# Kernel tuning notes

Hardware: AMD Instinct MI355X
Metric: run time of the kernel (lower is better)

The kernel has to match this reference:

```python
import jax, jax.numpy as jnp
import numpy as np

N_HEAD = 8
N_FEAT = 512
EPS = 1e-6


def _forward(query, Wq, bq, Wk, bk, Wv, bv, Wo, bo):
    # query: (bsz, tgt_len, E). key = value = query (self-attention).
    bsz, tgt_len, E = query.shape
    head_dim = E // N_HEAD
    n = bsz * N_HEAD

    # Faithful to torch: .view((L, N, E)) is a RESHAPE, not a transpose.
    x = query.reshape(tgt_len, bsz, E)

    q = x @ Wq.T + bq
    k = x @ Wk.T + bk
    v = x @ Wv.T + bv

    # relu activation on q, k (act_fun='relu')
    q = jax.nn.relu(q).reshape(tgt_len, n, head_dim).swapaxes(0, 1)  # (n, L, d)
    k = jax.nn.relu(k).reshape(tgt_len, n, head_dim).swapaxes(0, 1)  # (n, L, d)
    v = v.reshape(tgt_len, n, head_dim).swapaxes(0, 1)               # (n, L, d)

    # cos reweighting: weight_index = pi/2 * arange(1, m+1) / m
    m = tgt_len
    idx = (np.pi / 2) * jnp.arange(1, m + 1, dtype=query.dtype) / m  # (L,)
    idx = idx[None, :, None]                                         # (1, L, 1)
    q_ = jnp.concatenate([q * jnp.sin(idx), q * jnp.cos(idx)], axis=-1)  # (n, L, 2d)
    k_ = jnp.concatenate([k * jnp.sin(idx), k * jnp.cos(idx)], axis=-1)  # (n, L, 2d)

    # causal linear attention via cumsum recurrence
    kv = jnp.einsum('nld,nlm->nldm', k_, v)          # (n, L, 2d, d)
    kv_cum = jnp.cumsum(kv, axis=1)                  # (n, L, 2d, d)
    qkv = jnp.einsum('nld,nldm->nlm', q_, kv_cum)    # (n, L, d)
    k_cum = jnp.cumsum(k_, axis=1)                   # (n, L, 2d)
    denom = jnp.clip(jnp.einsum('nld,nld->nl', q_, k_cum), EPS, None)
    attn = qkv / denom[..., None]                    # (n, L, d)

    attn = attn.swapaxes(0, 1).reshape(tgt_len, bsz, E)
    out = attn @ Wo.T + bo
    # Faithful to torch: final .view back to (bsz, tgt_len, E) is a reshape.
    return out.reshape(bsz, tgt_len, N_FEAT)


def setup_inputs() -> dict:
    key = jax.random.key(0)
    ks = jax.random.split(key, 9)
    bsz, L, E = 2, 1024, N_FEAT
    scale = 0.02
    return {
        'query': jax.random.normal(ks[0], (bsz, L, E), dtype=jnp.float32),
        'Wq': jax.random.normal(ks[1], (E, E), dtype=jnp.float32) * scale,
        'bq': jnp.zeros((E,), dtype=jnp.float32),
        'Wk': jax.random.normal(ks[2], (E, E), dtype=jnp.float32) * scale,
        'bk': jnp.zeros((E,), dtype=jnp.float32),
        'Wv': jax.random.normal(ks[3], (E, E), dtype=jnp.float32) * scale,
        'bv': jnp.zeros((E,), dtype=jnp.float32),
        'Wo': jax.random.normal(ks[4], (E, E), dtype=jnp.float32) * scale,
        'bo': jnp.zeros((E,), dtype=jnp.float32),
    }


def reference(query, Wq, bq, Wk, bk, Wv, bv, Wo, bo):
    return _forward(query, Wq, bq, Wk, bk, Wv, bv, Wo, bo)
```

## Files before the change

### kernel.cpp

```cpp
#include <hip/hip_runtime.h>
#include <math.h>

#define LSEQ 1024
#define EDIM 512
#define HD 64
#define CCH 32
#define NCH 32
#define DFEAT 128

typedef unsigned short u16;
typedef short bf16x8 __attribute__((ext_vector_type(8)));
typedef float f32x4 __attribute__((ext_vector_type(4)));

__device__ __forceinline__ u16 f2bf(float f) {
    unsigned u = __float_as_uint(f);
    unsigned r = (u + 0x7fffu + ((u >> 16) & 1u)) >> 16;
    return (u16)r;
}
__device__ __forceinline__ float bf2f(u16 x) {
    return __uint_as_float((unsigned)x << 16);
}
__device__ __forceinline__ void async16(void* lds, const void* g) {
    __builtin_amdgcn_global_load_lds(
        (const __attribute__((address_space(1))) unsigned int*)g,
        (__attribute__((address_space(3))) unsigned int*)lds, 16, 0, 0);
}

__global__ __launch_bounds__(256) void cast_kernel(
    const float* __restrict__ X,  const float* __restrict__ Wq,
    const float* __restrict__ Wk, const float* __restrict__ Wv,
    const float* __restrict__ Wo, u16* __restrict__ Xb, u16* __restrict__ Wb)
{
    int i = blockIdx.x * 256 + threadIdx.x;
    const float* src; u16* dst; int off;
    if (i < 262144)      { src = X;  dst = Xb;          off = i; }
    else if (i < 327680) { src = Wq; dst = Wb;          off = i - 262144; }
    else if (i < 393216) { src = Wk; dst = Wb + 262144; off = i - 327680; }
    else if (i < 458752) { src = Wv; dst = Wb + 524288; off = i - 393216; }
    else                 { src = Wo; dst = Wb + 786432; off = i - 458752; }
    float4 v = *(const float4*)&src[(size_t)off * 4];
    ushort4 o; o.x = f2bf(v.x); o.y = f2bf(v.y); o.z = f2bf(v.z); o.w = f2bf(v.w);
    *(ushort4*)&dst[(size_t)off * 4] = o;
}

__global__ __launch_bounds__(256) void qkv_mfma_kernel(
    const u16* __restrict__ Xb, const u16* __restrict__ Wb,
    const float* __restrict__ bq, const float* __restrict__ bk, const float* __restrict__ bv,
    u16* __restrict__ qf, u16* __restrict__ kf, u16* __restrict__ vf)
{
    const int z = blockIdx.z;
    const u16* __restrict__ W = Wb + (size_t)z * 262144;
    const float* __restrict__ bias = (z == 0) ? bq : (z == 1) ? bk : bv;
    const int r0 = blockIdx.x * 128;
    const int j0 = blockIdx.y * 128;
    __shared__ u16 As[128 * 32];
    __shared__ u16 Bs[128 * 32];
    const int t = threadIdx.x;
    const int wave = t >> 6, lane = t & 63;
    const int wm = (wave & 1) * 64, wn = (wave >> 1) * 64;
    const int cl = lane & 15, rg4 = lane >> 4;
    f32x4 acc[4][4];
    #pragma unroll
    for (int fi = 0; fi < 4; ++fi)
        #pragma unroll
        for (int fj = 0; fj < 4; ++fj) acc[fi][fj] = (f32x4){0.f, 0.f, 0.f, 0.f};

    for (int kb = 0; kb < 512; kb += 32) {
        #pragma unroll
        for (int i = 0; i < 2; ++i) {
            int chunk = i * 256 + t;
            int row = chunk >> 2, kg = chunk & 3;
            async16(&As[(size_t)(i * 256 + wave * 64) * 8], Xb + (size_t)(r0 + row) * 512 + kb + kg * 8);
            async16(&Bs[(size_t)(i * 256 + wave * 64) * 8], W  + (size_t)(j0 + row) * 512 + kb + kg * 8);
        }
        __syncthreads();
        bf16x8 af[4], bg[4];
        #pragma unroll
        for (int f = 0; f < 4; ++f) {
            af[f] = *(const bf16x8*)&As[(wm + f * 16 + cl) * 32 + rg4 * 8];
            bg[f] = *(const bf16x8*)&Bs[(wn + f * 16 + cl) * 32 + rg4 * 8];
        }
        #pragma unroll
        for (int fi = 0; fi < 4; ++fi)
            #pragma unroll
            for (int fj = 0; fj < 4; ++fj)
                acc[fi][fj] = __builtin_amdgcn_mfma_f32_16x16x32_bf16(af[fi], bg[fj], acc[fi][fj], 0, 0, 0);
        __syncthreads();
    }

    float biasv[4];
    #pragma unroll
    for (int fj = 0; fj < 4; ++fj) biasv[fj] = bias[j0 + wn + fj * 16 + cl];
    #pragma unroll
    for (int fi = 0; fi < 4; ++fi) {
        #pragma unroll
        for (int rr = 0; rr < 4; ++rr) {
            const int row_g = r0 + wm + fi * 16 + rg4 * 4 + rr;
            const int l = row_g >> 1, bb = row_g & 1;
            if (z < 2) {
                float ang = 1.5707963267948966f * (float)(l + 1) * (1.0f / 1024.0f);
                float sv, cv;
                sincosf(ang, &sv, &cv);
                u16* __restrict__ dst = (z == 0) ? qf : kf;
                #pragma unroll
                for (int fj = 0; fj < 4; ++fj) {
                    const int jg = j0 + wn + fj * 16 + cl;
                    float y = fmaxf(acc[fi][fj][rr] + biasv[fj], 0.f);
                    const int h = jg >> 6, d = jg & 63;
                    size_t base = (size_t)((bb * 8 + h) * LSEQ + l) * DFEAT;
                    dst[base + d]      = f2bf(y * sv);
                    dst[base + d + 64] = f2bf(y * cv);
                }
            } else {
                #pragma unroll
                for (int fj = 0; fj < 4; ++fj) {
                    const int jg = j0 + wn + fj * 16 + cl;
                    float y = acc[fi][fj][rr] + biasv[fj];
                    const int h = jg >> 6, d = jg & 63;
                    vf[(size_t)((bb * 8 + h) * LSEQ + l) * HD + d] = f2bf(y);
                }
            }
        }
    }
}

__global__ __launch_bounds__(256) void chunk_sum_kernel(
    const u16* __restrict__ kf, const u16* __restrict__ vf,
    float* __restrict__ KVc, float* __restrict__ K1c)
{
    const int n = blockIdx.x >> 5;
    const int c = blockIdx.x & 31;
    __shared__ u16 Ks[32 * 128];
    __shared__ u16 VT[64 * 32];
    const int t = threadIdx.x;
    const int wave = t >> 6, lane = t & 63;
    const int cl = lane & 15, rg4 = lane >> 4;
    const u16* kbase = kf + (size_t)(n * LSEQ + c * CCH) * DFEAT;
    const u16* vbase = vf + (size_t)(n * LSEQ + c * CCH) * HD;
    #pragma unroll
    for (int i = 0; i < 2; ++i)
        async16(&Ks[(size_t)(i * 256 + wave * 64) * 8], kbase + (size_t)(i * 256 + t) * 8);
    {
        u16 tmp[8];
        #pragma unroll
        for (int j = 0; j < 8; ++j) tmp[j] = vbase[(wave * 8 + j) * HD + lane];
        *(bf16x8*)&VT[lane * 32 + wave * 8] = *(bf16x8*)tmp;
    }
    __syncthreads();

    bf16x8 af = *(const bf16x8*)&VT[(wave * 16 + cl) * 32 + rg4 * 8];
    f32x4 acc[8];
    #pragma unroll
    for (int ni = 0; ni < 8; ++ni) {
        u16 bt[8];
        #pragma unroll
        for (int j = 0; j < 8; ++j)
            bt[j] = Ks[(rg4 * 8 + j) * 128 + ni * 16 + cl];
        acc[ni] = __builtin_amdgcn_mfma_f32_16x16x32_bf16(af, *(bf16x8*)bt,
                                                          (f32x4){0.f,0.f,0.f,0.f}, 0, 0, 0);
    }
    float* out = KVc + (size_t)(n * NCH + c) * (HD * DFEAT);
    #pragma unroll
    for (int ni = 0; ni < 8; ++ni)
        #pragma unroll
        for (int r = 0; r < 4; ++r) {
            int m = wave * 16 + rg4 * 4 + r;
            out[(size_t)m * 128 + ni * 16 + cl] = acc[ni][r];
        }
    if (t < 128) {
        float s = 0.f;
        #pragma unroll
        for (int l = 0; l < 32; ++l) s += bf2f(Ks[l * 128 + t]);
        K1c[(size_t)(n * NCH + c) * DFEAT + t] = s;
    }
}

__global__ __launch_bounds__(256) void prefix_kernel(
    const float* __restrict__ KVc, const float* __restrict__ K1c,
    u16* __restrict__ Spt, float* __restrict__ K1p)
{
    const int bx = blockIdx.x, t = threadIdx.x;
    if (bx < 512) {
        const int n = bx >> 5;
        const int e = (bx & 31) * 256 + t;
        const float* src = KVc + (size_t)n * NCH * 8192 + e;
        u16* dst = Spt + (size_t)n * NCH * 8192 + e;
        float v[32];
        #pragma unroll
        for (int c = 0; c < 32; ++c) v[c] = src[(size_t)c * 8192];
        float run = 0.f;
        #pragma unroll
        for (int c = 0; c < 32; ++c) { dst[(size_t)c * 8192] = f2bf(run); run += v[c]; }
    } else {
        const int idx = (bx - 512) * 256 + t;
        const int n = idx >> 7, d = idx & 127;
        const float* src = K1c + (size_t)n * NCH * DFEAT + d;
        float* dst = K1p + (size_t)n * NCH * DFEAT + d;
        float v[32];
        #pragma unroll
        for (int c = 0; c < 32; ++c) v[c] = src[c * DFEAT];
        float run = 0.f;
        #pragma unroll
        for (int c = 0; c < 32; ++c) { dst[c * DFEAT] = run; run += v[c]; }
    }
}

__global__ __launch_bounds__(256) void attn_kernel(
    const u16* __restrict__ qf, const u16* __restrict__ kf, const u16* __restrict__ vf,
    const u16* __restrict__ Spt, const float* __restrict__ K1p,
    u16* __restrict__ Amb)
{
    const int n = blockIdx.x >> 5;
    const int c = blockIdx.x & 31;
    __shared__ u16 Qs[32 * 136];
    __shared__ u16 Ks[32 * 136];
    __shared__ u16 VT[64 * 32];
    __shared__ u16 Am[32 * 32];
    __shared__ float K1s[128];
    __shared__ float dsum2[2][32];
    __shared__ float qk1[32];
    const int t = threadIdx.x;
    const int wave = t >> 6, lane = t & 63;
    const int cl = lane & 15, rg4 = lane >> 4;
    const int mi = wave >> 1, nh = wave & 1;

    const u16* qbase = qf + (size_t)(n * LSEQ + c * CCH) * DFEAT;
    const u16* kbase = kf + (size_t)(n * LSEQ + c * CCH) * DFEAT;
    const u16* vbase = vf + (size_t)(n * LSEQ + c * CCH) * HD;
    const u16* spbase = Spt + (size_t)(n * NCH + c) * 8192;

    bf16x8 spf[2][4];
    #pragma unroll
    for (int ni2 = 0; ni2 < 2; ++ni2)
        #pragma unroll
        for (int ks = 0; ks < 4; ++ks)
            spf[ni2][ks] = *(const bf16x8*)&spbase[((2 * nh + ni2) * 16 + cl) * 128 + ks * 32 + rg4 * 8];

    #pragma unroll
    for (int i = 0; i < 2; ++i) {
        int chunk = i * 256 + t;
        int row = chunk >> 4, c8 = chunk & 15;
        *(bf16x8*)&Qs[row * 136 + c8 * 8] = *(const bf16x8*)&qbase[row * 128 + c8 * 8];
        *(bf16x8*)&Ks[row * 136 + c8 * 8] = *(const bf16x8*)&kbase[row * 128 + c8 * 8];
    }
    {
        u16 tmp[8];
        #pragma unroll
        for (int j = 0; j < 8; ++j) tmp[j] = vbase[(wave * 8 + j) * HD + lane];
        *(bf16x8*)&VT[lane * 32 + wave * 8] = *(bf16x8*)tmp;
    }
    if (t < 128) K1s[t] = K1p[(size_t)(n * NCH + c) * DFEAT + t];
    __syncthreads();

    f32x4 a_acc = (f32x4){0.f, 0.f, 0.f, 0.f};
    #pragma unroll
    for (int ks = 0; ks < 4; ++ks) {
        bf16x8 aq = *(const bf16x8*)&Qs[(mi * 16 + cl) * 136 + ks * 32 + rg4 * 8];
        bf16x8 bk = *(const bf16x8*)&Ks[(nh * 16 + cl) * 136 + ks * 32 + rg4 * 8];
        a_acc = __builtin_amdgcn_mfma_f32_16x16x32_bf16(aq, bk, a_acc, 0, 0, 0);
    }
    #pragma unroll
    for (int r = 0; r < 4; ++r) {
        int l_loc = mi * 16 + rg4 * 4 + r;
        int lp_loc = nh * 16 + cl;
        float v = (lp_loc <= l_loc) ? a_acc[r] : 0.f;
        Am[l_loc * 32 + lp_loc] = f2bf(v);
        float s = v;
        s += __shfl_xor(s, 1); s += __shfl_xor(s, 2);
        s += __shfl_xor(s, 4); s += __shfl_xor(s, 8);
        if (cl == 0) dsum2[nh][l_loc] = s;
    }
    {
        int row = wave * 8 + (lane >> 3), seg = lane & 7;
        float s = 0.f;
        #pragma unroll
        for (int j = 0; j < 16; ++j) {
            int d = seg * 16 + j;
            s += bf2f(Qs[row * 136 + d]) * K1s[d];
        }
        s += __shfl_xor(s, 1); s += __shfl_xor(s, 2); s += __shfl_xor(s, 4);
        if (seg == 0) qk1[row] = s;
    }
    __syncthreads();

    f32x4 oacc[2] = {(f32x4){0.f,0.f,0.f,0.f}, (f32x4){0.f,0.f,0.f,0.f}};
    #pragma unroll
    for (int ks = 0; ks < 4; ++ks) {
        bf16x8 aq = *(const bf16x8*)&Qs[(mi * 16 + cl) * 136 + ks * 32 + rg4 * 8];
        #pragma unroll
        for (int ni2 = 0; ni2 < 2; ++ni2)
            oacc[ni2] = __builtin_amdgcn_mfma_f32_16x16x32_bf16(aq, spf[ni2][ks], oacc[ni2], 0, 0, 0);
    }
    {
        bf16x8 aa = *(const bf16x8*)&Am[(mi * 16 + cl) * 32 + rg4 * 8];
        #pragma unroll
        for (int ni2 = 0; ni2 < 2; ++ni2) {
            bf16x8 bv = *(const bf16x8*)&VT[((2 * nh + ni2) * 16 + cl) * 32 + rg4 * 8];
            oacc[ni2] = __builtin_amdgcn_mfma_f32_16x16x32_bf16(aa, bv, oacc[ni2], 0, 0, 0);
        }
    }
    const int bb = n >> 3, h = n & 7;
    #pragma unroll
    for (int r = 0; r < 4; ++r) {
        int l_loc = mi * 16 + rg4 * 4 + r;
        float den = fmaxf(dsum2[0][l_loc] + dsum2[1][l_loc] + qk1[l_loc], 1e-6f);
        float inv = 1.0f / den;
        int rrow = (c * CCH + l_loc) * 2 + bb;
        #pragma unroll
        for (int ni2 = 0; ni2 < 2; ++ni2) {
            int m = (2 * nh + ni2) * 16 + cl;
            Amb[(size_t)rrow * EDIM + h * 64 + m] = f2bf(oacc[ni2][r] * inv);
        }
    }
}

__global__ __launch_bounds__(256) void out_mfma_kernel(
    const u16* __restrict__ Amb, const u16* __restrict__ Wob,
    const float* __restrict__ bo, float* __restrict__ out)
{
    const int r0 = blockIdx.x * 128;
    const int j0 = blockIdx.y * 128;
    __shared__ u16 As[128 * 32];
    __shared__ u16 Bs[128 * 32];
    const int t = threadIdx.x;
    const int wave = t >> 6, lane = t & 63;
    const int wm = (wave & 1) * 64, wn = (wave >> 1) * 64;
    const int cl = lane & 15, rg4 = lane >> 4;
    f32x4 acc[4][4];
    #pragma unroll
    for (int fi = 0; fi < 4; ++fi)
        #pragma unroll
        for (int fj = 0; fj < 4; ++fj) acc[fi][fj] = (f32x4){0.f, 0.f, 0.f, 0.f};

    for (int kb = 0; kb < 512; kb += 32) {
        #pragma unroll
        for (int i = 0; i < 2; ++i) {
            int chunk = i * 256 + t;
            int row = chunk >> 2, kg = chunk & 3;
            async16(&As[(size_t)(i * 256 + wave * 64) * 8], Amb + (size_t)(r0 + row) * 512 + kb + kg * 8);
            async16(&Bs[(size_t)(i * 256 + wave * 64) * 8], Wob + (size_t)(j0 + row) * 512 + kb + kg * 8);
        }
        __syncthreads();
        bf16x8 af[4], bg[4];
        #pragma unroll
        for (int f = 0; f < 4; ++f) {
            af[f] = *(const bf16x8*)&As[(wm + f * 16 + cl) * 32 + rg4 * 8];
            bg[f] = *(const bf16x8*)&Bs[(wn + f * 16 + cl) * 32 + rg4 * 8];
        }
        #pragma unroll
        for (int fi = 0; fi < 4; ++fi)
            #pragma unroll
            for (int fj = 0; fj < 4; ++fj)
                acc[fi][fj] = __builtin_amdgcn_mfma_f32_16x16x32_bf16(af[fi], bg[fj], acc[fi][fj], 0, 0, 0);
        __syncthreads();
    }

    float bov[4];
    #pragma unroll
    for (int fj = 0; fj < 4; ++fj) bov[fj] = bo[j0 + wn + fj * 16 + cl];
    #pragma unroll
    for (int fi = 0; fi < 4; ++fi)
        #pragma unroll
        for (int rr = 0; rr < 4; ++rr) {
            const int row_g = r0 + wm + fi * 16 + rg4 * 4 + rr;
            #pragma unroll
            for (int fj = 0; fj < 4; ++fj)
                out[(size_t)row_g * EDIM + j0 + wn + fj * 16 + cl] = acc[fi][fj][rr] + bov[fj];
        }
}

extern "C" void kernel_launch(void* const* d_in, const int* in_sizes, int n_in,
                              void* d_out, int out_size, void* d_ws, size_t ws_size,
                              hipStream_t stream) {
    const float* X  = (const float*)d_in[0];
    const float* Wq = (const float*)d_in[1]; const float* bq = (const float*)d_in[2];
    const float* Wk = (const float*)d_in[3]; const float* bk = (const float*)d_in[4];
    const float* Wv = (const float*)d_in[5]; const float* bv = (const float*)d_in[6];
    const float* Wo = (const float*)d_in[7]; const float* bo = (const float*)d_in[8];
    float* out = (float*)d_out;
    char* base = (char*)d_ws;
    u16*   qf  = (u16*)(base + 0);
    u16*   kf  = (u16*)(base + 4194304);
    u16*   vf  = (u16*)(base + 8388608);
    float* KVc = (float*)(base + 10485760);
    float* K1c = (float*)(base + 27262976);
    u16*   Spt = (u16*)(base + 27525120);
    float* K1p = (float*)(base + 35913728);
    u16*   Amb = (u16*)(base + 36175872);
    u16*   Xb  = (u16*)(base + 38273024);
    u16*   Wb  = (u16*)(base + 40370176);

    hipLaunchKernelGGL(cast_kernel, dim3(2048), dim3(256), 0, stream,
                       X, Wq, Wk, Wv, Wo, Xb, Wb);
    hipLaunchKernelGGL(qkv_mfma_kernel, dim3(16, 4, 3), dim3(256), 0, stream,
                       Xb, Wb, bq, bk, bv, qf, kf, vf);
    hipLaunchKernelGGL(chunk_sum_kernel, dim3(512), dim3(256), 0, stream, kf, vf, KVc, K1c);
    hipLaunchKernelGGL(prefix_kernel, dim3(520), dim3(256), 0, stream, KVc, K1c, Spt, K1p);
    hipLaunchKernelGGL(attn_kernel, dim3(512), dim3(256), 0, stream,
                       qf, kf, vf, Spt, K1p, Amb);
    hipLaunchKernelGGL(out_mfma_kernel, dim3(16, 4), dim3(256), 0, stream,
                       Amb, Wb + 786432, bo, out);
}
```

Before: 119.4 us.

## Shrink GEMM tiles, store chunk KV sums in bf16, transpose K/V in LDS

The QKV projection tile shrinks to 128x64 and the output projection to 64x64, so more blocks are launched across the CUs. The chunk-sum kernel now stages V via async LDS loads and transposes K in LDS, giving vectorized MFMA operand reads. Per-chunk KV sums are written as bf16 instead of fp32, halving that intermediate's traffic. The prefix kernel's K1 scan is folded into the first 8 blocks. This trades smaller tiles with less operand reuse and extra bf16 rounding in the prefix sums for more parallelism and less memory traffic.

```diff
diff --git a/kernel.cpp b/kernel.cpp
--- a/kernel.cpp
+++ b/kernel.cpp
@@ -52,72 +52,74 @@
     const u16* __restrict__ W = Wb + (size_t)z * 262144;
     const float* __restrict__ bias = (z == 0) ? bq : (z == 1) ? bk : bv;
     const int r0 = blockIdx.x * 128;
-    const int j0 = blockIdx.y * 128;
+    const int j0 = blockIdx.y * 64;
     __shared__ u16 As[128 * 32];
-    __shared__ u16 Bs[128 * 32];
+    __shared__ u16 Bs[64 * 32];
     const int t = threadIdx.x;
     const int wave = t >> 6, lane = t & 63;
-    const int wm = (wave & 1) * 64, wn = (wave >> 1) * 64;
     const int cl = lane & 15, rg4 = lane >> 4;
-    f32x4 acc[4][4];
-    #pragma unroll
-    for (int fi = 0; fi < 4; ++fi)
-        #pragma unroll
-        for (int fj = 0; fj < 4; ++fj) acc[fi][fj] = (f32x4){0.f, 0.f, 0.f, 0.f};
+    f32x4 acc[2][4];
+    #pragma unroll
+    for (int ri = 0; ri < 2; ++ri)
+        #pragma unroll
+        for (int cj = 0; cj < 4; ++cj) acc[ri][cj] = (f32x4){0.f, 0.f, 0.f, 0.f};
 
     for (int kb = 0; kb < 512; kb += 32) {
         #pragma unroll
         for (int i = 0; i < 2; ++i) {
             int chunk = i * 256 + t;
             int row = chunk >> 2, kg = chunk & 3;
-            async16(&As[(size_t)(i * 256 + wave * 64) * 8], Xb + (size_t)(r0 + row) * 512 + kb + kg * 8);
-            async16(&Bs[(size_t)(i * 256 + wave * 64) * 8], W  + (size_t)(j0 + row) * 512 + kb + kg * 8);
+            async16(&As[(i * 256 + wave * 64) * 8], Xb + (size_t)(r0 + row) * 512 + kb + kg * 8);
+        }
+        {
+            int row = t >> 2, kg = t & 3;
+            async16(&Bs[(wave * 64) * 8], W + (size_t)(j0 + row) * 512 + kb + kg * 8);
         }
         __syncthreads();
-        bf16x8 af[4], bg[4];
-        #pragma unroll
-        for (int f = 0; f < 4; ++f) {
-            af[f] = *(const bf16x8*)&As[(wm + f * 16 + cl) * 32 + rg4 * 8];
-            bg[f] = *(const bf16x8*)&Bs[(wn + f * 16 + cl) * 32 + rg4 * 8];
-        }
-        #pragma unroll
-        for (int fi = 0; fi < 4; ++fi)
+        bf16x8 af[2], bg[4];
+        #pragma unroll
+        for (int ri = 0; ri < 2; ++ri)
+            af[ri] = *(const bf16x8*)&As[(wave * 32 + ri * 16 + cl) * 32 + rg4 * 8];
+        #pragma unroll
+        for (int cj = 0; cj < 4; ++cj)
+            bg[cj] = *(const bf16x8*)&Bs[(cj * 16 + cl) * 32 + rg4 * 8];
+        #pragma unroll
+        for (int ri = 0; ri < 2; ++ri)
             #pragma unroll
-            for (int fj = 0; fj < 4; ++fj)
-                acc[fi][fj] = __builtin_amdgcn_mfma_f32_16x16x32_bf16(af[fi], bg[fj], acc[fi][fj], 0, 0, 0);
+            for (int cj = 0; cj < 4; ++cj)
+                acc[ri][cj] = __builtin_amdgcn_mfma_f32_16x16x32_bf16(af[ri], bg[cj], acc[ri][cj], 0, 0, 0);
         __syncthreads();
     }
 
     float biasv[4];
     #pragma unroll
-    for (int fj = 0; fj < 4; ++fj) biasv[fj] = bias[j0 + wn + fj * 16 + cl];
-    #pragma unroll
-    for (int fi = 0; fi < 4; ++fi) {
+    for (int cj = 0; cj < 4; ++cj) biasv[cj] = bias[j0 + cj * 16 + cl];
+    const int h = j0 >> 6;
+    #pragma unroll
+    for (int ri = 0; ri < 2; ++ri) {
         #pragma unroll
         for (int rr = 0; rr < 4; ++rr) {
-            const int row_g = r0 + wm + fi * 16 + rg4 * 4 + rr;
+            const int row_g = r0 + wave * 32 + ri * 16 + rg4 * 4 + rr;
             const int l = row_g >> 1, bb = row_g & 1;
             if (z < 2) {
                 float ang = 1.5707963267948966f * (float)(l + 1) * (1.0f / 1024.0f);
                 float sv, cv;
                 sincosf(ang, &sv, &cv);
                 u16* __restrict__ dst = (z == 0) ? qf : kf;
+                size_t base = (size_t)((bb * 8 + h) * LSEQ + l) * DFEAT;
                 #pragma unroll
-                for (int fj = 0; fj < 4; ++fj) {
-                    const int jg = j0 + wn + fj * 16 + cl;
-                    float y = fmaxf(acc[fi][fj][rr] + biasv[fj], 0.f);
-                    const int h = jg >> 6, d = jg & 63;
-                    size_t base = (size_t)((bb * 8 + h) * LSEQ + l) * DFEAT;
+                for (int cj = 0; cj < 4; ++cj) {
+                    const int d = cj * 16 + cl;
+                    float y = fmaxf(acc[ri][cj][rr] + biasv[cj], 0.f);
                     dst[base + d]      = f2bf(y * sv);
                     dst[base + d + 64] = f2bf(y * cv);
                 }
             } else {
+                size_t base = (size_t)((bb * 8 + h) * LSEQ + l) * HD;
                 #pragma unroll
-                for (int fj = 0; fj < 4; ++fj) {
-                    const int jg = j0 + wn + fj * 16 + cl;
-                    float y = acc[fi][fj][rr] + biasv[fj];
-                    const int h = jg >> 6, d = jg & 63;
-                    vf[(size_t)((bb * 8 + h) * LSEQ + l) * HD + d] = f2bf(y);
+                for (int cj = 0; cj < 4; ++cj) {
+                    const int d = cj * 16 + cl;
+                    vf[base + d] = f2bf(acc[ri][cj][rr] + biasv[cj]);
                 }
             }
         }
@@ -126,11 +128,13 @@
 
 __global__ __launch_bounds__(256) void chunk_sum_kernel(
     const u16* __restrict__ kf, const u16* __restrict__ vf,
-    float* __restrict__ KVc, float* __restrict__ K1c)
+    u16* __restrict__ KVc, float* __restrict__ K1c)
 {
     const int n = blockIdx.x >> 5;
     const int c = blockIdx.x & 31;
     __shared__ u16 Ks[32 * 128];
+    __shared__ u16 KT[128 * 32];
+    __shared__ u16 Vs[32 * 64];
     __shared__ u16 VT[64 * 32];
     const int t = threadIdx.x;
     const int wave = t >> 6, lane = t & 63;
@@ -139,69 +143,78 @@
     const u16* vbase = vf + (size_t)(n * LSEQ + c * CCH) * HD;
     #pragma unroll
     for (int i = 0; i < 2; ++i)
-        async16(&Ks[(size_t)(i * 256 + wave * 64) * 8], kbase + (size_t)(i * 256 + t) * 8);
+        async16(&Ks[(i * 256 + wave * 64) * 8], kbase + (size_t)(i * 256 + t) * 8);
+    async16(&Vs[(wave * 64) * 8], vbase + (size_t)t * 8);
+    __syncthreads();
     {
+        int m = t & 63, l0 = (t >> 6) * 8;
         u16 tmp[8];
         #pragma unroll
-        for (int j = 0; j < 8; ++j) tmp[j] = vbase[(wave * 8 + j) * HD + lane];
-        *(bf16x8*)&VT[lane * 32 + wave * 8] = *(bf16x8*)tmp;
+        for (int j = 0; j < 8; ++j) tmp[j] = Vs[(l0 + j) * 64 + m];
+        *(bf16x8*)&VT[m * 32 + l0] = *(bf16x8*)tmp;
+    }
+    {
+        int d = t & 127, l0 = (t >> 7) * 16;
+        #pragma unroll
+        for (int half = 0; half < 2; ++half) {
+            u16 tmp[8];
+            #pragma unroll
+            for (int j = 0; j < 8; ++j) tmp[j] = Ks[(l0 + half * 8 + j) * 128 + d];
+            *(bf16x8*)&KT[d * 32 + l0 + half * 8] = *(bf16x8*)tmp;
+        }
     }
     __syncthreads();
-
     bf16x8 af = *(const bf16x8*)&VT[(wave * 16 + cl) * 32 + rg4 * 8];
     f32x4 acc[8];
     #pragma unroll
     for (int ni = 0; ni < 8; ++ni) {
-        u16 bt[8];
-        #pragma unroll
-        for (int j = 0; j < 8; ++j)
-            bt[j] = Ks[(rg4 * 8 + j) * 128 + ni * 16 + cl];
-        acc[ni] = __builtin_amdgcn_mfma_f32_16x16x32_bf16(af, *(bf16x8*)bt,
-                                                          (f32x4){0.f,0.f,0.f,0.f}, 0, 0, 0);
-    }
-    float* out = KVc + (size_t)(n * NCH + c) * (HD * DFEAT);
+        bf16x8 bfr = *(const bf16x8*)&KT[(ni * 16 + cl) * 32 + rg4 * 8];
+        acc[ni] = __builtin_amdgcn_mfma_f32_16x16x32_bf16(af, bfr, (f32x4){0.f,0.f,0.f,0.f}, 0, 0, 0);
+    }
+    u16* outp = KVc + (size_t)(n * NCH + c) * (HD * DFEAT);
     #pragma unroll
     for (int ni = 0; ni < 8; ++ni)
         #pragma unroll
-        for (int r = 0; r < 4; ++r) {
-            int m = wave * 16 + rg4 * 4 + r;
-            out[(size_t)m * 128 + ni * 16 + cl] = acc[ni][r];
-        }
+        for (int r = 0; r < 4; ++r)
+            outp[(size_t)(wave * 16 + rg4 * 4 + r) * 128 + ni * 16 + cl] = f2bf(acc[ni][r]);
     if (t < 128) {
         float s = 0.f;
         #pragma unroll
-        for (int l = 0; l < 32; ++l) s += bf2f(Ks[l * 128 + t]);
+        for (int g = 0; g < 4; ++g) {
+            bf16x8 kv = *(const bf16x8*)&KT[t * 32 + g * 8];
+            #pragma unroll
+            for (int j = 0; j < 8; ++j) s += bf2f(((u16*)&kv)[j]);
+        }
         K1c[(size_t)(n * NCH + c) * DFEAT + t] = s;
     }
 }
 
 __global__ __launch_bounds__(256) void prefix_kernel(
-    const float* __restrict__ KVc, const float* __restrict__ K1c,
+    const u16* __restrict__ KVc, const float* __restrict__ K1c,
     u16* __restrict__ Spt, float* __restrict__ K1p)
 {
-    const int bx = blockIdx.x, t = threadIdx.x;
-    if (bx < 512) {
-        const int n = bx >> 5;
-        const int e = (bx & 31) * 256 + t;
-        const float* src = KVc + (size_t)n * NCH * 8192 + e;
-        u16* dst = Spt + (size_t)n * NCH * 8192 + e;
-        float v[32];
-        #pragma unroll
-        for (int c = 0; c < 32; ++c) v[c] = src[(size_t)c * 8192];
-        float run = 0.f;
-        #pragma unroll
-        for (int c = 0; c < 32; ++c) { dst[(size_t)c * 8192] = f2bf(run); run += v[c]; }
-    } else {
-        const int idx = (bx - 512) * 256 + t;
-        const int n = idx >> 7, d = idx & 127;
-        const float* src = K1c + (size_t)n * NCH * DFEAT + d;
-        float* dst = K1p + (size_t)n * NCH * DFEAT + d;
-        float v[32];
-        #pragma unroll
-        for (int c = 0; c < 32; ++c) v[c] = src[c * DFEAT];
-        float run = 0.f;
-        #pragma unroll
-        for (int c = 0; c < 32; ++c) { dst[c * DFEAT] = run; run += v[c]; }
+    const int b = blockIdx.x, t = threadIdx.x;
+    const int n = b >> 5;
+    const int e = (b & 31) * 256 + t;
+    const u16* src = KVc + (size_t)n * NCH * 8192 + e;
+    u16* dst = Spt + (size_t)n * NCH * 8192 + e;
+    float v[32];
+    #pragma unroll
+    for (int cc = 0; cc < 32; ++cc) v[cc] = bf2f(src[(size_t)cc * 8192]);
+    float run = 0.f;
+    #pragma unroll
+    for (int cc = 0; cc < 32; ++cc) { dst[(size_t)cc * 8192] = f2bf(run); run += v[cc]; }
+    if (b < 8) {
+        const int idx = b * 256 + t;
+        const int nn = idx >> 7, d = idx & 127;
+        const float* s2 = K1c + (size_t)nn * NCH * DFEAT + d;
+        float* d2 = K1p + (size_t)nn * NCH * DFEAT + d;
+        float v2[32];
+        #pragma unroll
+        for (int cc = 0; cc < 32; ++cc) v2[cc] = s2[cc * DFEAT];
+        float run2 = 0.f;
+        #pragma unroll
+        for (int cc = 0; cc < 32; ++cc) { d2[cc * DFEAT] = run2; run2 += v2[cc]; }
     }
 }
 
@@ -318,55 +331,45 @@
     const u16* __restrict__ Amb, const u16* __restrict__ Wob,
     const float* __restrict__ bo, float* __restrict__ out)
 {
-    const int r0 = blockIdx.x * 128;
-    const int j0 = blockIdx.y * 128;
-    __shared__ u16 As[128 * 32];
-    __shared__ u16 Bs[128 * 32];
+    const int r0 = blockIdx.x * 64;
+    const int j0 = blockIdx.y * 64;
+    __shared__ u16 As[64 * 32];
+    __shared__ u16 Bs[64 * 32];
     const int t = threadIdx.x;
     const int wave = t >> 6, lane = t & 63;
-    const int wm = (wave & 1) * 64, wn = (wave >> 1) * 64;
     const int cl = lane & 15, rg4 = lane >> 4;
-    f32x4 acc[4][4];
-    #pragma unroll
-    for (int fi = 0; fi < 4; ++fi)
-        #pragma unroll
-        for (int fj = 0; fj < 4; ++fj) acc[fi][fj] = (f32x4){0.f, 0.f, 0.f, 0.f};
+    f32x4 acc[4];
+    #pragma unroll
+    for (int cj = 0; cj < 4; ++cj) acc[cj] = (f32x4){0.f, 0.f, 0.f, 0.f};
 
     for (int kb = 0; kb < 512; kb += 32) {
-        #pragma unroll
-        for (int i = 0; i < 2; ++i) {
-            int chunk = i * 256 + t;
-            int row = chunk >> 2, kg = chunk & 3;
-            async16(&As[(size_t)(i * 256 + wave * 64) * 8], Amb + (size_t)(r0 + row) * 512 + kb + kg * 8);
-            async16(&Bs[(size_t)(i * 256 + wave * 64) * 8], Wob + (size_t)(j0 + row) * 512 + kb + kg * 8);
+        {
+            int row = t >> 2, kg = t & 3;
+            async16(&As[(wave * 64) * 8], Amb + (size_t)(r0 + row) * 512 + kb + kg * 8);
+            async16(&Bs[(wave * 64) * 8], Wob + (size_t)(j0 + row) * 512 + kb + kg * 8);
         }
         __syncthreads();
-        bf16x8 af[4], bg[4];
-        #pragma unroll
-        for (int f = 0; f < 4; ++f) {
-            af[f] = *(const bf16x8*)&As[(wm + f * 16 + cl) * 32 + rg4 * 8];
-            bg[f] = *(const bf16x8*)&Bs[(wn + f * 16 + cl) * 32 + rg4 * 8];
-        }
-        #pragma unroll
-        for (int fi = 0; fi < 4; ++fi)
-            #pragma unroll
-            for (int fj = 0; fj < 4; ++fj)
-                acc[fi][fj] = __builtin_amdgcn_mfma_f32_16x16x32_bf16(af[fi], bg[fj], acc[fi][fj], 0, 0, 0);
+        bf16x8 af = *(const bf16x8*)&As[(wave * 16 + cl) * 32 + rg4 * 8];
+        bf16x8 bg[4];
+        #pragma unroll
+        for (int cj = 0; cj < 4; ++cj)
+            bg[cj] = *(const bf16x8*)&Bs[(cj * 16 + cl) * 32 + rg4 * 8];
+        #pragma unroll
+        for (int cj = 0; cj < 4; ++cj)
+            acc[cj] = __builtin_amdgcn_mfma_f32_16x16x32_bf16(af, bg[cj], acc[cj], 0, 0, 0);
         __syncthreads();
     }
 
     float bov[4];
     #pragma unroll
-    for (int fj = 0; fj < 4; ++fj) bov[fj] = bo[j0 + wn + fj * 16 + cl];
-    #pragma unroll
-    for (int fi = 0; fi < 4; ++fi)
-        #pragma unroll
-        for (int rr = 0; rr < 4; ++rr) {
-            const int row_g = r0 + wm + fi * 16 + rg4 * 4 + rr;
-            #pragma unroll
-            for (int fj = 0; fj < 4; ++fj)
-                out[(size_t)row_g * EDIM + j0 + wn + fj * 16 + cl] = acc[fi][fj][rr] + bov[fj];
-        }
+    for (int cj = 0; cj < 4; ++cj) bov[cj] = bo[j0 + cj * 16 + cl];
+    #pragma unroll
+    for (int rr = 0; rr < 4; ++rr) {
+        const int row_g = r0 + wave * 16 + rg4 * 4 + rr;
+        #pragma unroll
+        for (int cj = 0; cj < 4; ++cj)
+            out[(size_t)row_g * EDIM + j0 + cj * 16 + cl] = acc[cj][rr] + bov[cj];
+    }
 }
 
 extern "C" void kernel_launch(void* const* d_in, const int* in_sizes, int n_in,
@@ -382,22 +385,22 @@
     u16*   qf  = (u16*)(base + 0);
     u16*   kf  = (u16*)(base + 4194304);
     u16*   vf  = (u16*)(base + 8388608);
-    float* KVc = (float*)(base + 10485760);
-    float* K1c = (float*)(base + 27262976);
-    u16*   Spt = (u16*)(base + 27525120);
-    float* K1p = (float*)(base + 35913728);
-    u16*   Amb = (u16*)(base + 36175872);
-    u16*   Xb  = (u16*)(base + 38273024);
-    u16*   Wb  = (u16*)(base + 40370176);
+    u16*   KVc = (u16*)(base + 10485760);
+    float* K1c = (float*)(base + 18874368);
+    u16*   Spt = (u16*)(base + 19136512);
+    float* K1p = (float*)(base + 27525120);
+    u16*   Amb = (u16*)(base + 27787264);
+    u16*   Xb  = (u16*)(base + 29884416);
+    u16*   Wb  = (u16*)(base + 31981568);
 
     hipLaunchKernelGGL(cast_kernel, dim3(2048), dim3(256), 0, stream,
                        X, Wq, Wk, Wv, Wo, Xb, Wb);
-    hipLaunchKernelGGL(qkv_mfma_kernel, dim3(16, 4, 3), dim3(256), 0, stream,
+    hipLaunchKernelGGL(qkv_mfma_kernel, dim3(16, 8, 3), dim3(256), 0, stream,
                        Xb, Wb, bq, bk, bv, qf, kf, vf);
     hipLaunchKernelGGL(chunk_sum_kernel, dim3(512), dim3(256), 0, stream, kf, vf, KVc, K1c);
-    hipLaunchKernelGGL(prefix_kernel, dim3(520), dim3(256), 0, stream, KVc, K1c, Spt, K1p);
+    hipLaunchKernelGGL(prefix_kernel, dim3(512), dim3(256), 0, stream, KVc, K1c, Spt, K1p);
     hipLaunchKernelGGL(attn_kernel, dim3(512), dim3(256), 0, stream,
                        qf, kf, vf, Spt, K1p, Amb);
-    hipLaunchKernelGGL(out_mfma_kernel, dim3(16, 4), dim3(256), 0, stream,
+    hipLaunchKernelGGL(out_mfma_kernel, dim3(32, 8), dim3(256), 0, stream,
                        Amb, Wb + 786432, bo, out);
 }
```

New measurement: 111.0 us. -7.1%, faster.
